# Optimization experiments

Hardware: AMD Instinct MI355X
Metric: run time of the kernel (lower is better)

## Reference

```python
import jax, jax.numpy as jnp
import numpy as np

NHEAD = 16


def setup_inputs() -> dict:
    key = jax.random.key(0)
    ks = jax.random.split(key, 9)
    d = 1024
    scale = 0.03  # keep projected q,k in a sane range (like trained weights)
    return {
        "x": jax.random.normal(ks[0], (4, 4096, d), jnp.float32),
        "wq": jax.random.normal(ks[1], (d, d), jnp.float32) * scale,
        "bq": jax.random.normal(ks[2], (d,), jnp.float32) * scale,
        "wk": jax.random.normal(ks[3], (d, d), jnp.float32) * scale,
        "bk": jax.random.normal(ks[4], (d,), jnp.float32) * scale,
        "wv": jax.random.normal(ks[5], (d, d), jnp.float32) * scale,
        "bv": jax.random.normal(ks[6], (d,), jnp.float32) * scale,
        "wo": jax.random.normal(ks[7], (d, d), jnp.float32) * scale,
        "bo": jax.random.normal(ks[8], (d,), jnp.float32) * scale,
        "window_size": 128,
    }


def reference(x, wq, bq, wk, bk, wv, bv, wo, bo, window_size):
    B, S, D = x.shape
    H = NHEAD
    Dh = D // H
    w = int(window_size)

    def proj(wm, b):
        # [B,S,D] -> [B,H,S,Dh]
        return (x @ wm.T + b).reshape(B, S, H, Dh).transpose(0, 2, 1, 3)

    q = proj(wq, bq)
    k = proj(wk, bk)
    v = proj(wv, bv)

    # Pad K/V along seq so offset slices are static-size [B,H,S,Dh].
    Kp = jnp.pad(k, ((0, 0), (0, 0), (w, w), (0, 0)))
    Vp = jnp.pad(v, ((0, 0), (0, 0), (w, w), (0, 0)))
    pos = jnp.arange(S)
    inv_sqrt = np.float32(1.0 / np.sqrt(Dh))

    # Faithful to the Triton kernel: a sequential scan over window offsets with a
    # RUNNING max but NO rescaling of the accumulators (the kernel's exact math).
    def step(carry, t):
        m, o_acc, t_acc = carry
        kj = jax.lax.dynamic_slice_in_dim(Kp, t, S, axis=2)  # key at offset t-w
        vj = jax.lax.dynamic_slice_in_dim(Vp, t, S, axis=2)
        s = jnp.einsum("bhsd,bhsd->bhs", q, kj) * inv_sqrt
        j = pos + t - w
        valid = (j >= 0) & (j < S)  # [S], broadcasts over [B,H,S]
        m_new = jnp.where(valid, jnp.maximum(m, s), m)
        p = jnp.exp(jnp.where(valid, s - m_new, -jnp.inf))  # 0 where invalid
        return (m_new, o_acc + p[..., None] * vj, t_acc + p), None

    init = (
        jnp.full((B, H, S), -jnp.inf, dtype=x.dtype),
        jnp.zeros((B, H, S, Dh), dtype=x.dtype),
        jnp.zeros((B, H, S), dtype=x.dtype),
    )
    (m, o_acc, t_acc), _ = jax.lax.scan(step, init, jnp.arange(2 * w + 1))
    o = o_acc / t_acc[..., None]  # [B,H,S,Dh]
    out = o.transpose(0, 2, 1, 3).reshape(B, S, D)
    return out @ wo.T + bo
```

## Files before the change

### kernel.cpp

```cpp
#include <hip/hip_runtime.h>
#include <math.h>

#define S_LEN  4096
#define BATCH  4
#define DMODEL 1024
#define NHEADS 16
#define DHEAD  64
#define WIN    128

typedef _Float16 half8   __attribute__((ext_vector_type(8)));
typedef _Float16 half4_t __attribute__((ext_vector_type(4)));
typedef float    floatx4 __attribute__((ext_vector_type(4)));

__device__ __forceinline__ void gload16(const void* g, void* l) {
    __builtin_amdgcn_global_load_lds(
        (const __attribute__((address_space(1))) void*)g,
        (__attribute__((address_space(3))) void*)l, 16, 0, 0);
}

__global__ __launch_bounds__(256)
void cvt_f32_f16(const float4* __restrict__ in, half4_t* __restrict__ out, int n4) {
    for (int i = blockIdx.x * blockDim.x + threadIdx.x; i < n4;
         i += gridDim.x * blockDim.x) {
        const float4 a = in[i];
        half4_t h;
        h[0] = (_Float16)a.x; h[1] = (_Float16)a.y;
        h[2] = (_Float16)a.z; h[3] = (_Float16)a.w;
        out[i] = h;
    }
}

__global__ __launch_bounds__(256)
void cvt4_f32_f16(const float4* __restrict__ w0, const float4* __restrict__ w1,
                  const float4* __restrict__ w2, const float4* __restrict__ w3,
                  half4_t* __restrict__ o0, half4_t* __restrict__ o1,
                  half4_t* __restrict__ o2, half4_t* __restrict__ o3, int n4) {
    const float4* in  = blockIdx.y == 0 ? w0 : (blockIdx.y == 1 ? w1 : (blockIdx.y == 2 ? w2 : w3));
    half4_t*      out = blockIdx.y == 0 ? o0 : (blockIdx.y == 1 ? o1 : (blockIdx.y == 2 ? o2 : o3));
    for (int i = blockIdx.x * blockDim.x + threadIdx.x; i < n4;
         i += gridDim.x * blockDim.x) {
        const float4 a = in[i];
        half4_t h;
        h[0] = (_Float16)a.x; h[1] = (_Float16)a.y;
        h[2] = (_Float16)a.z; h[3] = (_Float16)a.w;
        out[i] = h;
    }
}

template<int MODE, int NTN>
__global__ __launch_bounds__(512)
void gemm8p(const _Float16* __restrict__ A, const _Float16* __restrict__ W,
            const float* __restrict__ B0, const float* __restrict__ B1,
            const float* __restrict__ B2, void* __restrict__ out_base)
{
    constexpr int K  = DMODEL;
    constexpr int nt = K / 64;
    const int bid  = blockIdx.x;
    const int nwg8 = (64 * NTN) >> 3;
    const int swz  = (bid & 7) * nwg8 + (bid >> 3);
    const int i0   = (swz / NTN) * 256;
    const int n0   = (swz % NTN) * 256;

    __shared__ _Float16 As[4][128 * 64];
    __shared__ _Float16 Bs[4][128 * 64];

    const int tid  = threadIdx.x;
    const int lane = tid & 63;
    const int wid  = tid >> 6;
    const int wr   = wid >> 2;
    const int wc   = wid & 3;
    const int fr   = lane & 15;
    const int fh   = lane >> 4;
    const int sw8  = fr & 7;
    const int ok0  = ((fh) ^ sw8) * 8;
    const int ok1  = ((4 + fh) ^ sw8) * 8;
    const int arow = (wr * 16 + fr) * 64;
    const int brow = (wc * 16 + fr) * 64;

    const int srow = tid >> 3;
    const int ssw  = ((tid & 7) ^ (srow & 7)) << 3;
    const _Float16* baseA = A + (size_t)(i0 + srow) * K + ssw;
    const _Float16* baseB = W + (size_t)(n0 + srow) * K + ssw;
    const int ldso = tid * 8;

    floatx4 acc[8][4];
    #pragma unroll
    for (int mi = 0; mi < 8; ++mi)
        #pragma unroll
        for (int ni = 0; ni < 4; ++ni) acc[mi][ni] = (floatx4)0.f;

    half8 a_lo[4][2], a_hi[4][2], b_lo[2][2], b_hi[2][2];

#define ST_A(TT, H)                                                          \
    do {                                                                     \
        _Float16* d_ = &As[(((TT) & 1) << 1) | (H)][ldso];                   \
        const _Float16* s_ = baseA + (size_t)((H) * 128) * K + (TT) * 64;    \
        gload16(s_, d_);                                                     \
        gload16(s_ + (size_t)64 * K, d_ + 4096);                             \
    } while (0)
#define ST_B(TT, H)                                                          \
    do {                                                                     \
        _Float16* d_ = &Bs[(((TT) & 1) << 1) | (H)][ldso];                   \
        const _Float16* s_ = baseB + (size_t)((H) * 128) * K + (TT) * 64;    \
        gload16(s_, d_);                                                     \
        gload16(s_ + (size_t)64 * K, d_ + 4096);                             \
    } while (0)
#define RD_A(DST, DB, H)                                                     \
    _Pragma("unroll")                                                        \
    for (int mi = 0; mi < 4; ++mi) {                                         \
        DST[mi][0] = *(const half8*)&As[(DB) | (H)][arow + mi * 2048 + ok0]; \
        DST[mi][1] = *(const half8*)&As[(DB) | (H)][arow + mi * 2048 + ok1]; \
    }
#define RD_B(DST, DB, H)                                                     \
    _Pragma("unroll")                                                        \
    for (int ni = 0; ni < 2; ++ni) {                                         \
        DST[ni][0] = *(const half8*)&Bs[(DB) | (H)][brow + ni * 4096 + ok0]; \
        DST[ni][1] = *(const half8*)&Bs[(DB) | (H)][brow + ni * 4096 + ok1]; \
    }
#define MFMA16(MB, NB, AA, BB)                                               \
    __builtin_amdgcn_s_setprio(1);                                           \
    _Pragma("unroll")                                                        \
    for (int kc = 0; kc < 2; ++kc)                                           \
        _Pragma("unroll")                                                    \
        for (int mi = 0; mi < 4; ++mi)                                       \
            _Pragma("unroll")                                                \
            for (int ni = 0; ni < 2; ++ni)                                   \
                acc[MB + mi][NB + ni] = __builtin_amdgcn_mfma_f32_16x16x32_f16( \
                    AA[mi][kc], BB[ni][kc], acc[MB + mi][NB + ni], 0, 0, 0); \
    __builtin_amdgcn_s_setprio(0);
#define PHEND                                                                \
    asm volatile("s_waitcnt lgkmcnt(0)" ::: "memory");                       \
    __builtin_amdgcn_sched_barrier(0);                                       \
    __builtin_amdgcn_s_barrier();

    ST_A(0, 0); ST_B(0, 0); ST_B(0, 1); ST_A(0, 1);
    ST_A(1, 0); ST_B(1, 1); ST_A(1, 1); ST_B(1, 0);
    asm volatile("s_waitcnt vmcnt(8)" ::: "memory");
    __builtin_amdgcn_sched_barrier(0);
    __builtin_amdgcn_s_barrier();
    RD_A(a_lo, 0, 0); RD_B(b_lo, 0, 0);
    asm volatile("s_waitcnt lgkmcnt(0)" ::: "memory");
    __builtin_amdgcn_sched_barrier(0);

    for (int t = 0; t < nt; ++t) {
        const int d2 = (t & 1) << 1;
        const bool st = (t + 2) < nt;
        RD_B(b_hi, d2, 1);
        MFMA16(0, 0, a_lo, b_lo);
        PHEND;
        RD_A(a_hi, d2, 1);
        if (st) { ST_B(t + 2, 1); ST_A(t + 2, 0); }
        MFMA16(0, 2, a_lo, b_hi);
        PHEND;
        if (st) ST_A(t + 2, 1);
        MFMA16(4, 2, a_hi, b_hi);
        PHEND;
        if (st) ST_B(t + 2, 0);
        MFMA16(4, 0, a_hi, b_lo);
        if (st) {
            asm volatile("s_waitcnt vmcnt(8)" ::: "memory");
        } else if (t + 1 < nt) {
            asm volatile("s_waitcnt vmcnt(0)" ::: "memory");
        }
        __builtin_amdgcn_sched_barrier(0);
        __builtin_amdgcn_s_barrier();
        if (t + 1 < nt) {
            const int dn = ((t + 1) & 1) << 1;
            RD_A(a_lo, dn, 0); RD_B(b_lo, dn, 0);
            asm volatile("s_waitcnt lgkmcnt(0)" ::: "memory");
            __builtin_amdgcn_sched_barrier(0);
        }
    }
#undef ST_A
#undef ST_B
#undef RD_A
#undef RD_B
#undef MFMA16
#undef PHEND

    const int z  = (MODE == 0) ? (n0 >> 10) : 0;
    const float* bz = (MODE == 1) ? B0 : (z == 0 ? B0 : (z == 1 ? B1 : B2));

    #pragma unroll
    for (int ni = 0; ni < 4; ++ni) {
        const int gc   = n0 + ni * 64 + wc * 16 + fr;
        const int gcol = gc & (DMODEL - 1);
        const float bv = bz[gcol];
        #pragma unroll
        for (int mi = 0; mi < 8; ++mi) {
            const int gr = i0 + mi * 32 + wr * 16 + fh * 4;
            const floatx4 v = acc[mi][ni];
            if (MODE == 0) {
                _Float16* outh = (_Float16*)out_base
                               + (size_t)z * ((size_t)16384 * DMODEL);
                const int bb = gr >> 12;
                const int sp = gr & (S_LEN - 1);
                const int hh = gcol >> 6;
                const int dh = gcol & 63;
                if (z < 2) {
                    #pragma unroll
                    for (int r = 0; r < 4; ++r)
                        outh[((((size_t)(bb * NHEADS + hh)) * S_LEN + sp + r) << 6) + dh] =
                            (_Float16)(v[r] + bv);
                } else {
                    half4_t hv;
                    hv[0] = (_Float16)(v[0] + bv); hv[1] = (_Float16)(v[1] + bv);
                    hv[2] = (_Float16)(v[2] + bv); hv[3] = (_Float16)(v[3] + bv);
                    *(half4_t*)&outh[(((size_t)(bb * NHEADS + hh)) * DHEAD + dh) * S_LEN + sp] = hv;
                }
            } else {
                float* out = (float*)out_base;
                #pragma unroll
                for (int r = 0; r < 4; ++r)
                    out[(size_t)(gr + r) * DMODEL + gcol] = v[r] + bv;
            }
        }
    }
}

__global__ __launch_bounds__(256)
void attn_mfma(const _Float16* __restrict__ qh_, const _Float16* __restrict__ kh_,
               const _Float16* __restrict__ vth_, _Float16* __restrict__ o)
{
    __shared__ __align__(16) _Float16 Qs[64 * 64];
    __shared__ __align__(16) _Float16 Ks[64 * 64];
    __shared__ __align__(16) _Float16 Vt[64 * 64];
    __shared__ __align__(16) float    SP[64 * 68];
    __shared__ __align__(16) _Float16 P16[64 * 64];
    __shared__ float CM[64 * 4];
    __shared__ float TSs[64 * 4];
    __shared__ float Mq[64];
    __shared__ float Tq[64];

    const int tid   = threadIdx.x;
    const int lane  = tid & 63;
    const int w     = tid >> 6;
    const int qbase = blockIdx.x * 64;
    const int head  = blockIdx.y, b = blockIdx.z;
    const size_t bh = (size_t)(b * NHEADS + head);

    const _Float16* qg = qh_  + bh * (size_t)(S_LEN * DHEAD);
    const _Float16* kg = kh_  + bh * (size_t)(S_LEN * DHEAD);
    const _Float16* vg = vth_ + bh * (size_t)(DHEAD * S_LEN);

    const int fr = lane & 15;
    const int fh = lane >> 4;

    #pragma unroll
    for (int rep = 0; rep < 2; ++rep) {
        const int c = tid + 256 * rep;
        const int row = c >> 3, sll = c & 7;
        gload16(qg + (size_t)(qbase + row) * 64 + (size_t)((sll ^ (row & 7)) * 8),
                Qs + (size_t)c * 8);
    }
    if (tid < 64) { Mq[tid] = -INFINITY; Tq[tid] = 0.f; }

    floatx4 Oacc[4];
    #pragma unroll
    for (int ni = 0; ni < 4; ++ni) Oacc[ni] = (floatx4)0.f;

    for (int c = 0; c < 5; ++c) {
        const int jlo = qbase - WIN + c * 64;
        if (jlo < 0 || jlo >= S_LEN) continue;
        const int base_rel = jlo - qbase + WIN;

        __syncthreads();

        #pragma unroll
        for (int rep = 0; rep < 2; ++rep) {
            const int cc = tid + 256 * rep;
            const int row = cc >> 3, sll = cc & 7;
            gload16(kg + (size_t)(jlo + row) * 64 + (size_t)((sll ^ (row & 7)) * 8),
                    Ks + (size_t)cc * 8);
            gload16(vg + (size_t)row * S_LEN + jlo + (size_t)((sll ^ (row & 7)) * 8),
                    Vt + (size_t)cc * 8);
        }
        __syncthreads();

        {
            floatx4 acc[4];
            #pragma unroll
            for (int ni = 0; ni < 4; ++ni) acc[ni] = (floatx4)0.f;
            half8 a[2];
            #pragma unroll
            for (int kc = 0; kc < 2; ++kc) {
                const int row = 16 * w + fr;
                a[kc] = *(const half8*)&Qs[row * 64 + ((fh + 4 * kc) ^ (row & 7)) * 8];
            }
            #pragma unroll
            for (int ni = 0; ni < 4; ++ni)
                #pragma unroll
                for (int kc = 0; kc < 2; ++kc) {
                    const int tr = 16 * ni + fr;
                    half8 bf = *(const half8*)&Ks[tr * 64 + ((fh + 4 * kc) ^ (tr & 7)) * 8];
                    acc[ni] = __builtin_amdgcn_mfma_f32_16x16x32_f16(a[kc], bf, acc[ni], 0, 0, 0);
                }
            #pragma unroll
            for (int ni = 0; ni < 4; ++ni)
                #pragma unroll
                for (int r = 0; r < 4; ++r)
                    SP[(16 * w + 4 * fh + r) * 68 + fr + 16 * ni] = acc[ni][r] * 0.125f;
        }
        __syncthreads();

        const int sq = lane;
        float sv[16], run[16];
        {
            float m_run = -INFINITY;
            #pragma unroll
            for (int u = 0; u < 4; ++u) {
                const float4 s4 = *(const float4*)&SP[sq * 68 + w * 16 + 4 * u];
                const float se[4] = {s4.x, s4.y, s4.z, s4.w};
                #pragma unroll
                for (int e = 0; e < 4; ++e) {
                    const int i = 4 * u + e;
                    const int rel = base_rel + 16 * w + i - sq;
                    const bool valid = (rel >= 0) && (rel <= 2 * WIN);
                    const float s = valid ? se[e] : -INFINITY;
                    sv[i] = s;
                    m_run = fmaxf(m_run, s);
                    run[i] = m_run;
                }
            }
            CM[sq * 4 + w] = m_run;
        }
        __syncthreads();

        {
            float pre = Mq[sq];
            if (w > 0) pre = fmaxf(pre, CM[sq * 4 + 0]);
            if (w > 1) pre = fmaxf(pre, CM[sq * 4 + 1]);
            if (w > 2) pre = fmaxf(pre, CM[sq * 4 + 2]);
            float tl = 0.f;
            _Float16 pf[16];
            #pragma unroll
            for (int i = 0; i < 16; ++i) {
                const float wv = fmaxf(pre, run[i]);
                const float p = (sv[i] != -INFINITY) ? __expf(sv[i] - wv) : 0.f;
                tl += p;
                pf[i] = (_Float16)p;
            }
            TSs[sq * 4 + w] = tl;
            #pragma unroll
            for (int u = 0; u < 2; ++u) {
                half8 h8;
                #pragma unroll
                for (int e = 0; e < 8; ++e) h8[e] = pf[8 * u + e];
                *(half8*)&P16[sq * 64 + ((2 * w + u) ^ (sq & 7)) * 8] = h8;
            }
        }
        __syncthreads();

        if (tid < 64) {
            const float mm = fmaxf(fmaxf(CM[tid * 4 + 0], CM[tid * 4 + 1]),
                                   fmaxf(CM[tid * 4 + 2], CM[tid * 4 + 3]));
            Mq[tid] = fmaxf(Mq[tid], mm);
            Tq[tid] += TSs[tid * 4 + 0] + TSs[tid * 4 + 1] + TSs[tid * 4 + 2] + TSs[tid * 4 + 3];
        }

        {
            half8 pa[2];
            #pragma unroll
            for (int kc = 0; kc < 2; ++kc) {
                const int row = 16 * w + fr;
                pa[kc] = *(const half8*)&P16[row * 64 + ((fh + 4 * kc) ^ (row & 7)) * 8];
            }
            #pragma unroll
            for (int ni = 0; ni < 4; ++ni)
                #pragma unroll
                for (int kc = 0; kc < 2; ++kc) {
                    const int dr = 16 * ni + fr;
                    half8 bf = *(const half8*)&Vt[dr * 64 + ((fh + 4 * kc) ^ (dr & 7)) * 8];
                    Oacc[ni] = __builtin_amdgcn_mfma_f32_16x16x32_f16(pa[kc], bf, Oacc[ni], 0, 0, 0);
                }
        }
    }

    __syncthreads();

    #pragma unroll
    for (int ni = 0; ni < 4; ++ni)
        #pragma unroll
        for (int r = 0; r < 4; ++r) {
            const int q  = 16 * w + 4 * fh + r;
            const float inv = 1.0f / Tq[q];
            o[((size_t)(b * S_LEN + qbase + q) * NHEADS + head) * DHEAD + fr + 16 * ni] =
                (_Float16)(Oacc[ni][r] * inv);
        }
}

extern "C" void kernel_launch(void* const* d_in, const int* in_sizes, int n_in,
                              void* d_out, int out_size, void* d_ws, size_t ws_size,
                              hipStream_t stream) {
    const float* x  = (const float*)d_in[0];
    const float* wq = (const float*)d_in[1];
    const float* bq = (const float*)d_in[2];
    const float* wk = (const float*)d_in[3];
    const float* bk = (const float*)d_in[4];
    const float* wv = (const float*)d_in[5];
    const float* bv = (const float*)d_in[6];
    const float* wo = (const float*)d_in[7];
    const float* bo = (const float*)d_in[8];

    const size_t BUF = (size_t)BATCH * S_LEN * DMODEL;
    _Float16* xh  = (_Float16*)d_ws;
    _Float16* qh  = xh + BUF;
    _Float16* kh  = qh + BUF;
    _Float16* vth = kh + BUF;
    _Float16* oh  = vth + BUF;
    _Float16* wqh = oh + BUF;
    _Float16* wkh = wqh + DMODEL * DMODEL;
    _Float16* wvh = wkh + DMODEL * DMODEL;
    _Float16* woh = wvh + DMODEL * DMODEL;

    cvt_f32_f16<<<2048, 256, 0, stream>>>((const float4*)x, (half4_t*)xh, (int)(BUF / 4));
    cvt4_f32_f16<<<dim3(256, 4), 256, 0, stream>>>(
        (const float4*)wq, (const float4*)wk, (const float4*)wv, (const float4*)wo,
        (half4_t*)wqh, (half4_t*)wkh, (half4_t*)wvh, (half4_t*)woh,
        DMODEL * DMODEL / 4);

    gemm8p<0, 12><<<64 * 12, 512, 0, stream>>>(xh, wqh, bq, bk, bv, (void*)qh);

    dim3 gattn(S_LEN / 64, NHEADS, BATCH);
    attn_mfma<<<gattn, 256, 0, stream>>>(qh, kh, vth, oh);

    gemm8p<1, 4><<<64 * 4, 512, 0, stream>>>(oh, woh, bo, bo, bo, d_out);
}
```

Measured before the change: 254.1 us.

## Restructure GEMM main loop into three phases with double-buffered low fragments

Rewrites the GEMM k-loop from four barrier-separated phases into three, unrolling by two with ping-pong register fragment sets (a_l0/a_l1, b_l0/b_l1). The next tile's low fragments are read from LDS during the last MFMA phase instead of after a separate barrier. The intent is fewer barriers and more overlap of LDS reads with MFMA. The cost is higher register pressure, and correctness now depends on the waitcnt placement before reading the next buffer.

```diff
diff --git a/kernel.cpp b/kernel.cpp
--- a/kernel.cpp
+++ b/kernel.cpp
@@ -49,7 +49,7 @@
 
 template<int MODE, int NTN>
 __global__ __launch_bounds__(512)
-void gemm8p(const _Float16* __restrict__ A, const _Float16* __restrict__ W,
+void gemm3p(const _Float16* __restrict__ A, const _Float16* __restrict__ W,
             const float* __restrict__ B0, const float* __restrict__ B1,
             const float* __restrict__ B2, void* __restrict__ out_base)
 {
@@ -89,7 +89,8 @@
         #pragma unroll
         for (int ni = 0; ni < 4; ++ni) acc[mi][ni] = (floatx4)0.f;
 
-    half8 a_lo[4][2], a_hi[4][2], b_lo[2][2], b_hi[2][2];
+    half8 a_l0[4][2], a_l1[4][2], b_l0[2][2], b_l1[2][2];
+    half8 a_hi[4][2], b_hi[2][2];
 
 #define ST_A(TT, H)                                                          \
     do {                                                                     \
@@ -133,43 +134,43 @@
     __builtin_amdgcn_sched_barrier(0);                                       \
     __builtin_amdgcn_s_barrier();
 
-    ST_A(0, 0); ST_B(0, 0); ST_B(0, 1); ST_A(0, 1);
-    ST_A(1, 0); ST_B(1, 1); ST_A(1, 1); ST_B(1, 0);
+#define TILE_BODY(T, D2, DN, ALc, BLc, ALn, BLn)                             \
+    {                                                                        \
+        const bool st = (T) + 2 < nt;                                        \
+                                                             \
+        RD_B(b_hi, D2, 1);                                                   \
+        MFMA16(0, 0, ALc, BLc);                                              \
+        PHEND;                                                               \
+                                                             \
+        RD_A(a_hi, D2, 1);                                                   \
+        if (st) { ST_B((T) + 2, 1); ST_A((T) + 2, 0); }                      \
+        MFMA16(0, 2, ALc, b_hi);                                             \
+        PHEND;                                                               \
+                             \
+        if (st) { ST_A((T) + 2, 1); ST_B((T) + 2, 0); }                      \
+        if (st) {                                                            \
+            asm volatile("s_waitcnt vmcnt(8)" ::: "memory");                 \
+        } else if ((T) + 1 < nt) {                                           \
+            asm volatile("s_waitcnt vmcnt(0)" ::: "memory");                 \
+        }                                                                    \
+        if ((T) + 1 < nt) { RD_A(ALn, DN, 0); RD_B(BLn, DN, 0); }            \
+        MFMA16(4, 2, a_hi, b_hi);                                            \
+        MFMA16(4, 0, a_hi, BLc);                                             \
+        PHEND;                                                               \
+    }
+
+    ST_B(0, 1); ST_A(0, 0); ST_A(0, 1); ST_B(0, 0);
+    ST_B(1, 1); ST_A(1, 0); ST_A(1, 1); ST_B(1, 0);
     asm volatile("s_waitcnt vmcnt(8)" ::: "memory");
     __builtin_amdgcn_sched_barrier(0);
     __builtin_amdgcn_s_barrier();
-    RD_A(a_lo, 0, 0); RD_B(b_lo, 0, 0);
+    RD_A(a_l0, 0, 0); RD_B(b_l0, 0, 0);
     asm volatile("s_waitcnt lgkmcnt(0)" ::: "memory");
     __builtin_amdgcn_sched_barrier(0);
 
-    for (int t = 0; t < nt; ++t) {
-        const int d2 = (t & 1) << 1;
-        const bool st = (t + 2) < nt;
-        RD_B(b_hi, d2, 1);
-        MFMA16(0, 0, a_lo, b_lo);
-        PHEND;
-        RD_A(a_hi, d2, 1);
-        if (st) { ST_B(t + 2, 1); ST_A(t + 2, 0); }
-        MFMA16(0, 2, a_lo, b_hi);
-        PHEND;
-        if (st) ST_A(t + 2, 1);
-        MFMA16(4, 2, a_hi, b_hi);
-        PHEND;
-        if (st) ST_B(t + 2, 0);
-        MFMA16(4, 0, a_hi, b_lo);
-        if (st) {
-            asm volatile("s_waitcnt vmcnt(8)" ::: "memory");
-        } else if (t + 1 < nt) {
-            asm volatile("s_waitcnt vmcnt(0)" ::: "memory");
-        }
-        __builtin_amdgcn_sched_barrier(0);
-        __builtin_amdgcn_s_barrier();
-        if (t + 1 < nt) {
-            const int dn = ((t + 1) & 1) << 1;
-            RD_A(a_lo, dn, 0); RD_B(b_lo, dn, 0);
-            asm volatile("s_waitcnt lgkmcnt(0)" ::: "memory");
-            __builtin_amdgcn_sched_barrier(0);
-        }
+    for (int t = 0; t < nt; t += 2) {
+        TILE_BODY(t,     0, 2, a_l0, b_l0, a_l1, b_l1);
+        TILE_BODY(t + 1, 2, 0, a_l1, b_l1, a_l0, b_l0);
     }
 #undef ST_A
 #undef ST_B
@@ -177,6 +178,7 @@
 #undef RD_B
 #undef MFMA16
 #undef PHEND
+#undef TILE_BODY
 
     const int z  = (MODE == 0) ? (n0 >> 10) : 0;
     const float* bz = (MODE == 1) ? B0 : (z == 0 ? B0 : (z == 1 ? B1 : B2));
@@ -419,10 +421,10 @@
         (half4_t*)wqh, (half4_t*)wkh, (half4_t*)wvh, (half4_t*)woh,
         DMODEL * DMODEL / 4);
 
-    gemm8p<0, 12><<<64 * 12, 512, 0, stream>>>(xh, wqh, bq, bk, bv, (void*)qh);
+    gemm3p<0, 12><<<64 * 12, 512, 0, stream>>>(xh, wqh, bq, bk, bv, (void*)qh);
 
     dim3 gattn(S_LEN / 64, NHEADS, BATCH);
     attn_mfma<<<gattn, 256, 0, stream>>>(qh, kh, vth, oh);
 
-    gemm8p<1, 4><<<64 * 4, 512, 0, stream>>>(oh, woh, bo, bo, bo, d_out);
-}
+    gemm3p<1, 4><<<64 * 4, 512, 0, stream>>>(oh, woh, bo, bo, bo, d_out);
+}
```

Result: slower. 487.8 us (+92.0%).
